# Kernel tuning notes

Measured on AMD Instinct MI355X. Metric: run time of the kernel, lower is better.

Reference implementation:

```python
import jax, jax.numpy as jnp
import numpy as np

EPS = 1e-6
N, D = 8192, 256


def setup_inputs() -> dict:
    key = jax.random.key(0)
    kq, kc = jax.random.split(key)
    # scale 0.05 keeps points inside the Poincare ball: c*||q||^2 ~ 0.06 << 1
    query = jax.random.normal(kq, (N, D), dtype=jnp.float32) * 0.05
    c = jnp.asarray(0.1, dtype=jnp.float32)  # learnable curvature param (init 0.1)
    return {"query": query, "c": c}


def reference(query, c):
    # Self-attention path of HyperbolicAttention (keys = values = query).
    clamp_c = jnp.maximum(c, EPS)
    # ||u-v||^2 = ||u||^2 + ||v||^2 - 2 u.v  (same math as explicit expand+subtract,
    # but via a single GEMM instead of an (N, N, D) intermediate)
    qn = jnp.sum(query * query, axis=-1)                       # (N,)
    gram = query @ query.T                                     # (N, N)
    diff_sq = jnp.maximum(qn[:, None] + qn[None, :] - 2.0 * gram, 0.0)
    t = jnp.maximum(1.0 - clamp_c * qn, EPS)                   # clamped 1 - c||x||^2
    denom = t[:, None] * t[None, :]                            # (N, N)
    arg = jnp.maximum(1.0 + 2.0 * clamp_c * diff_sq / denom, 1.0 + EPS) + EPS
    dist = jnp.arccosh(arg) / jnp.sqrt(clamp_c)                # (N, N)
    attn = jax.nn.softmax(-dist, axis=-1)                      # (N, N)
    return attn @ query                                        # (N, D)
```

## Files before the change

### kernel.cpp

```cpp
#include <hip/hip_runtime.h>
#include <math.h>

#define NN 8192
#define DD 256
#define EPSV 1e-6f
#define BM 128
#define BN 64
#define CSPLIT 4
#define COLS_PER_BLOCK (NN / CSPLIT)
#define NJT (COLS_PER_BLOCK / BN)
#define PSTR 72
#define TSTR 266
#define SMEM_BYTES (32768 * 3 + BM * PSTR * 2)

typedef __bf16 bf16x8 __attribute__((ext_vector_type(8)));
typedef float f32x16 __attribute__((ext_vector_type(16)));
typedef unsigned short ushort;
typedef unsigned int uint;


__device__ inline ushort f2bf(float x) {
    uint u = __float_as_uint(x);
    u += 0x7fffu + ((u >> 16) & 1u);
    return (ushort)(u >> 16);
}

__device__ inline void gload_lds16(const void* g, void* l) {
    __builtin_amdgcn_global_load_lds((const __attribute__((address_space(1))) uint*)g,
                                     (__attribute__((address_space(3))) uint*)l, 16, 0, 0);
}

__global__ void zero_kernel(float* __restrict__ p) {
    int i = blockIdx.x * 256 + threadIdx.x;
    ((float4*)p)[i] = make_float4(0.f, 0.f, 0.f, 0.f);
}

__global__ void prep_kernel(const float* __restrict__ q, const float* __restrict__ cp,
                            ushort* __restrict__ qbf, ushort* __restrict__ qbfT,
                            float* __restrict__ qn, float* __restrict__ itv2) {
    __shared__ ushort T[64 * TSTR];
    const int t = threadIdx.x;
    const int p0 = blockIdx.x * 64;
    const int pr = t >> 2, fq = t & 3;
    const int row = p0 + pr;
    const float4* src = (const float4*)(q + (size_t)row * DD + fq * 64);
    ushort loc[64];
    float ss = 0.f;
    #pragma unroll
    for (int i = 0; i < 16; ++i) {
        float4 v = src[i];
        ushort b0 = f2bf(v.x), b1 = f2bf(v.y), b2 = f2bf(v.z), b3 = f2bf(v.w);
        loc[i * 4 + 0] = b0; loc[i * 4 + 1] = b1; loc[i * 4 + 2] = b2; loc[i * 4 + 3] = b3;
        float r0 = __uint_as_float((uint)b0 << 16), r1 = __uint_as_float((uint)b1 << 16);
        float r2 = __uint_as_float((uint)b2 << 16), r3 = __uint_as_float((uint)b3 << 16);
        ss += r0 * r0 + r1 * r1 + r2 * r2 + r3 * r3;
    }
    #pragma unroll
    for (int k = 0; k < 8; ++k)
        *(uint4*)(qbf + (size_t)row * DD + (((fq * 8 + k) ^ (row & 7)) * 8)) = *(uint4*)&loc[k * 8];
    #pragma unroll
    for (int k = 0; k < 32; ++k)
        *(ushort2*)&T[pr * TSTR + fq * 64 + k * 2] = *(ushort2*)&loc[k * 2];
    ss += __shfl_xor(ss, 1, 64);
    ss += __shfl_xor(ss, 2, 64);
    if (fq == 0) {
        float cc = fmaxf(cp[0], EPSV);
        qn[row] = ss;
        float tt = fmaxf(1.0f - cc * ss, EPSV);
        itv2[row] = sqrtf(2.0f * cc) / tt;
    }
    __syncthreads();
    #pragma unroll
    for (int pass = 0; pass < 4; ++pass) {
        int f = pass * 64 + (t >> 2);
        int quarter = t & 3;
        ushort tmp[16];
        #pragma unroll
        for (int i = 0; i < 16; ++i) tmp[i] = T[(quarter * 16 + i) * TSTR + f];
        *(uint4*)(qbfT + (size_t)f * NN + p0 + quarter * 16) = *(uint4*)&tmp[0];
        *(uint4*)(qbfT + (size_t)f * NN + p0 + quarter * 16 + 8) = *(uint4*)&tmp[8];
    }
}

__global__ __launch_bounds__(512, 2) void flash_kernel(
    const ushort* __restrict__ qbf, const ushort* __restrict__ qbfT,
    const float* __restrict__ cp, const float* __restrict__ qn,
    const float* __restrict__ itv2, float* __restrict__ Oacc, float* __restrict__ lacc) {
    extern __shared__ char smem[];
    ushort* Ktlds = (ushort*)(smem + 65536);
    ushort* Plds = (ushort*)(smem + 98304);

    const int tid = threadIdx.x;
    const int lane = tid & 63;
    const int w = tid >> 6;
    const int l31 = lane & 31;
    const int lhi = lane >> 5;
    const int qr = w >> 1;
    const int qc = w & 1;
    const int R0 = blockIdx.y * BM;
    const int C0 = blockIdx.x * COLS_PER_BLOCK;

    const float cc = fmaxf(cp[0], EPSV);
    const float rsc = rsqrtf(cc);

    const int rowA = R0 + qr * 32 + l31;
    const ushort* qrow = qbf + (size_t)rowA * DD;
    bf16x8 qa[16];
    #pragma unroll
    for (int kk = 0; kk < 16; ++kk) {
        int c = kk * 2 + lhi;
        qa[kk] = *(const bf16x8*)(qrow + ((c ^ (rowA & 7)) * 8));
    }

    float qnr16[16], itr16[16];
    #pragma unroll
    for (int r = 0; r < 16; ++r) {
        int row = R0 + qr * 32 + (r & 3) + 8 * (r >> 2) + 4 * lhi;
        qnr16[r] = qn[row];
        itr16[r] = itv2[row];
    }

    f32x16 o[4];
    #pragma unroll
    for (int ct = 0; ct < 4; ++ct)
        #pragma unroll
        for (int i = 0; i < 16; ++i) o[ct][i] = 0.f;
    float racc[16];
    #pragma unroll
    for (int r = 0; r < 16; ++r) racc[r] = 0.f;

    {
        const char* g = (const char*)(qbf + (size_t)C0 * DD);
        #pragma unroll
        for (int i = 0; i < 4; ++i) {
            int base = i * 8192 + w * 1024;
            gload_lds16(g + base + lane * 16, smem + base);
        }
    }

    #pragma unroll 1
    for (int jt = 0; jt < NJT; ++jt) {
        const int C = C0 + jt * BN;
        const ushort* Kc = (const ushort*)(smem + (jt & 1) * 32768);
        __syncthreads();

        if (jt + 1 < NJT) {
            const char* g = (const char*)(qbf + (size_t)(C + BN) * DD);
            char* dst = smem + ((jt + 1) & 1) * 32768;
            #pragma unroll
            for (int i = 0; i < 4; ++i) {
                int base = i * 8192 + w * 1024;
                gload_lds16(g + base + lane * 16, dst + base);
            }
        }
        {
            #pragma unroll
            for (int i = 0; i < 4; ++i) {
                int f0 = i * 64 + w * 8;
                int f = f0 + (lane >> 3);
                const char* g = (const char*)(qbfT + (size_t)f * NN + C) +
                                (((lane & 7) ^ (f & 7)) * 16);
                gload_lds16(g, (char*)Ktlds + f0 * 128);
            }
        }

        f32x16 s;
        #pragma unroll
        for (int i = 0; i < 16; ++i) s[i] = 0.f;
        const int jrow = qc * 32 + l31;
        const ushort* krow = Kc + jrow * DD;
        #pragma unroll
        for (int kk = 0; kk < 16; ++kk) {
            int c = kk * 2 + lhi;
            bf16x8 b = *(const bf16x8*)(krow + ((c ^ (jrow & 7)) * 8));
            s = __builtin_amdgcn_mfma_f32_32x32x16_bf16(qa[kk], b, s, 0, 0, 0);
        }

        {
            int J = C + jrow;
            float qnj = qn[J];
            float itj = itv2[J];
            #pragma unroll
            for (int r = 0; r < 16; ++r) {
                int mloc = qr * 32 + (r & 3) + 8 * (r >> 2) + 4 * lhi;
                float diff = fmaxf(qnr16[r] + qnj - 2.0f * s[r], 0.0f);
                float u = diff * itr16[r] * itj;
                float z = fmaxf(1.0f + u, 1.0f + EPSV) + EPSV;
                float y = z + sqrtf(fmaf(z, z, -1.0f));
                float p = __builtin_amdgcn_exp2f(-rsc * __builtin_amdgcn_logf(y));
                racc[r] += p;
                Plds[mloc * PSTR + jrow] = f2bf(p);
            }
        }
        __syncthreads();

        #pragma unroll
        for (int kt = 0; kt < 4; ++kt) {
            bf16x8 pa = *(const bf16x8*)&Plds[(qr * 32 + l31) * PSTR + kt * 16 + 8 * lhi];
            #pragma unroll
            for (int ct = 0; ct < 4; ++ct) {
                int f = qc * 128 + ct * 32 + l31;
                int cj = kt * 2 + lhi;
                bf16x8 vb = *(const bf16x8*)(Ktlds + f * 64 + (((cj ^ (f & 7))) * 8));
                o[ct] = __builtin_amdgcn_mfma_f32_32x32x16_bf16(pa, vb, o[ct], 0, 0, 0);
            }
        }
    }

    #pragma unroll
    for (int ct = 0; ct < 4; ++ct) {
        #pragma unroll
        for (int r = 0; r < 16; ++r) {
            int row = R0 + qr * 32 + (r & 3) + 8 * (r >> 2) + 4 * lhi;
            int d = qc * 128 + ct * 32 + l31;
            atomicAdd(&Oacc[(size_t)row * DD + d], o[ct][r]);
        }
    }
    #pragma unroll
    for (int off = 1; off <= 16; off <<= 1)
        #pragma unroll
        for (int r = 0; r < 16; ++r) racc[r] += __shfl_xor(racc[r], off, 64);
    if (l31 == 0) {
        #pragma unroll
        for (int r = 0; r < 16; ++r) {
            int row = R0 + qr * 32 + (r & 3) + 8 * (r >> 2) + 4 * lhi;
            atomicAdd(&lacc[row], racc[r]);
        }
    }
}

__global__ void norm_kernel(const float* __restrict__ Oacc, const float* __restrict__ lacc,
                            float* __restrict__ out) {
    int i = blockIdx.x * 256 + threadIdx.x;
    float4 v = ((const float4*)Oacc)[i];
    float inv = 1.0f / lacc[i >> 6];
    ((float4*)out)[i] = make_float4(v.x * inv, v.y * inv, v.z * inv, v.w * inv);
}

extern "C" void kernel_launch(void* const* d_in, const int* in_sizes, int n_in,
                              void* d_out, int out_size, void* d_ws, size_t ws_size,
                              hipStream_t stream) {
    (void)in_sizes; (void)n_in; (void)out_size; (void)ws_size;
    const float* q = (const float*)d_in[0];
    const float* cp = (const float*)d_in[1];
    float* out = (float*)d_out;
    float* ws = (float*)d_ws;
    float* Oacc = ws;
    float* lacc = ws + (size_t)NN * DD;
    float* qn = lacc + NN;
    float* itv2 = qn + NN;
    ushort* qbf = (ushort*)(itv2 + NN);
    ushort* qbfT = qbf + (size_t)NN * DD;

    (void)hipFuncSetAttribute((const void*)flash_kernel,
                              hipFuncAttributeMaxDynamicSharedMemorySize, SMEM_BYTES);

    zero_kernel<<<(NN * DD + NN) / 4 / 256, 256, 0, stream>>>(ws);
    prep_kernel<<<NN / 64, 256, 0, stream>>>(q, cp, qbf, qbfT, qn, itv2);
    flash_kernel<<<dim3(CSPLIT, NN / BM), 512, SMEM_BYTES, stream>>>(qbf, qbfT, cp, qn, itv2, Oacc, lacc);
    norm_kernel<<<(NN * DD / 4) / 256, 256, 0, stream>>>(Oacc, lacc, out);
}
```

Before: 205.6 us.

## Pre-tile bf16 operands in MFMA fragment order and read K/V directly from global

The prep kernel now writes the bf16 query and its transpose in blocked layouts matching MFMA fragment order, packs the norm and inverse-t values into one float2 array, and zeroes the accumulators itself so the separate zero kernel goes away. The flash kernel drops the LDS staging of K and V and reads fragments straight from global memory (relying on cache), transposes the score GEMM so each lane owns one query row, and passes P through a smaller double-buffered LDS region built with lane shuffles, removing one barrier per tile. The aim is less LDS traffic, fewer barriers and one fewer launch. The risk is that uncoalesced or poorly cached global fragment loads now sit on the critical path without any prefetch overlap.

```diff
diff --git a/kernel.cpp b/kernel.cpp
--- a/kernel.cpp
+++ b/kernel.cpp
@@ -9,9 +9,7 @@
 #define CSPLIT 4
 #define COLS_PER_BLOCK (NN / CSPLIT)
 #define NJT (COLS_PER_BLOCK / BN)
-#define PSTR 72
 #define TSTR 266
-#define SMEM_BYTES (32768 * 3 + BM * PSTR * 2)
 
 typedef __bf16 bf16x8 __attribute__((ext_vector_type(8)));
 typedef float f32x16 __attribute__((ext_vector_type(16)));
@@ -25,24 +23,20 @@
     return (ushort)(u >> 16);
 }
 
-__device__ inline void gload_lds16(const void* g, void* l) {
-    __builtin_amdgcn_global_load_lds((const __attribute__((address_space(1))) uint*)g,
-                                     (__attribute__((address_space(3))) uint*)l, 16, 0, 0);
-}
-
-__global__ void zero_kernel(float* __restrict__ p) {
-    int i = blockIdx.x * 256 + threadIdx.x;
-    ((float4*)p)[i] = make_float4(0.f, 0.f, 0.f, 0.f);
-}
-
 __global__ void prep_kernel(const float* __restrict__ q, const float* __restrict__ cp,
-                            ushort* __restrict__ qbf, ushort* __restrict__ qbfT,
-                            float* __restrict__ qn, float* __restrict__ itv2) {
+                            ushort* __restrict__ qbfA, ushort* __restrict__ qbfB,
+                            float2* __restrict__ qni,
+                            float* __restrict__ Oacc, float* __restrict__ lacc) {
     __shared__ ushort T[64 * TSTR];
     const int t = threadIdx.x;
-    const int p0 = blockIdx.x * 64;
+    const int b = blockIdx.x;
+    float4 z4 = make_float4(0.f, 0.f, 0.f, 0.f);
+    #pragma unroll
+    for (int i = 0; i < 16; ++i) ((float4*)Oacc)[b * 4096 + i * 256 + t] = z4;
+    if (t < 16) ((float4*)lacc)[b * 16 + t] = z4;
+
     const int pr = t >> 2, fq = t & 3;
-    const int row = p0 + pr;
+    const int row = b * 64 + pr;
     const float4* src = (const float4*)(q + (size_t)row * DD + fq * 64);
     ushort loc[64];
     float ss = 0.f;
@@ -57,7 +51,7 @@
     }
     #pragma unroll
     for (int k = 0; k < 8; ++k)
-        *(uint4*)(qbf + (size_t)row * DD + (((fq * 8 + k) ^ (row & 7)) * 8)) = *(uint4*)&loc[k * 8];
+        *(uint4*)(qbfA + (((size_t)b * 32 + fq * 8 + k) * 64 + pr) * 8) = *(uint4*)&loc[k * 8];
     #pragma unroll
     for (int k = 0; k < 32; ++k)
         *(ushort2*)&T[pr * TSTR + fq * 64 + k * 2] = *(ushort2*)&loc[k * 2];
@@ -65,9 +59,8 @@
     ss += __shfl_xor(ss, 2, 64);
     if (fq == 0) {
         float cc = fmaxf(cp[0], EPSV);
-        qn[row] = ss;
         float tt = fmaxf(1.0f - cc * ss, EPSV);
-        itv2[row] = sqrtf(2.0f * cc) / tt;
+        qni[row] = make_float2(ss, sqrtf(2.0f * cc) / tt);
     }
     __syncthreads();
     #pragma unroll
@@ -77,156 +70,129 @@
         ushort tmp[16];
         #pragma unroll
         for (int i = 0; i < 16; ++i) tmp[i] = T[(quarter * 16 + i) * TSTR + f];
-        *(uint4*)(qbfT + (size_t)f * NN + p0 + quarter * 16) = *(uint4*)&tmp[0];
-        *(uint4*)(qbfT + (size_t)f * NN + p0 + quarter * 16 + 8) = *(uint4*)&tmp[8];
+        *(uint4*)(qbfB + (((size_t)b * 8 + quarter * 2 + 0) * 256 + f) * 8) = *(uint4*)&tmp[0];
+        *(uint4*)(qbfB + (((size_t)b * 8 + quarter * 2 + 1) * 256 + f) * 8) = *(uint4*)&tmp[8];
     }
 }
 
 __global__ __launch_bounds__(512, 2) void flash_kernel(
-    const ushort* __restrict__ qbf, const ushort* __restrict__ qbfT,
-    const float* __restrict__ cp, const float* __restrict__ qn,
-    const float* __restrict__ itv2, float* __restrict__ Oacc, float* __restrict__ lacc) {
-    extern __shared__ char smem[];
-    ushort* Ktlds = (ushort*)(smem + 65536);
-    ushort* Plds = (ushort*)(smem + 98304);
+    const ushort* __restrict__ qbfA, const ushort* __restrict__ qbfB,
+    const float* __restrict__ cp, const float2* __restrict__ qni,
+    float* __restrict__ Oacc, float* __restrict__ lacc) {
+    __shared__ char px[32768];
 
     const int tid = threadIdx.x;
     const int lane = tid & 63;
     const int w = tid >> 6;
     const int l31 = lane & 31;
     const int lhi = lane >> 5;
-    const int qr = w >> 1;
-    const int qc = w & 1;
-    const int R0 = blockIdx.y * BM;
-    const int C0 = blockIdx.x * COLS_PER_BLOCK;
+    const int mr = w >> 1;
+    const int jh = w & 1;
+
+    const int lid = blockIdx.x;
+    const int cs = lid & 3;
+    const int rb = lid >> 2;
+    const int R0 = rb * BM;
+    const int jbC0 = cs * (COLS_PER_BLOCK / 64);
 
     const float cc = fmaxf(cp[0], EPSV);
-    const float rsc = rsqrtf(cc);
-
-    const int rowA = R0 + qr * 32 + l31;
-    const ushort* qrow = qbf + (size_t)rowA * DD;
+    const float nrsc = -rsqrtf(cc);
+
     bf16x8 qa[16];
-    #pragma unroll
-    for (int kk = 0; kk < 16; ++kk) {
-        int c = kk * 2 + lhi;
-        qa[kk] = *(const bf16x8*)(qrow + ((c ^ (rowA & 7)) * 8));
-    }
-
-    float qnr16[16], itr16[16];
-    #pragma unroll
-    for (int r = 0; r < 16; ++r) {
-        int row = R0 + qr * 32 + (r & 3) + 8 * (r >> 2) + 4 * lhi;
-        qnr16[r] = qn[row];
-        itr16[r] = itv2[row];
-    }
+    {
+        const int jbQ = (R0 >> 6) + (mr >> 1);
+        const int rl = (mr & 1) * 32 + l31;
+        #pragma unroll
+        for (int kk = 0; kk < 16; ++kk)
+            qa[kk] = *(const bf16x8*)(qbfA + (((size_t)jbQ * 32 + kk * 2 + lhi) * 64 + rl) * 8);
+    }
+    const float2 mv = qni[R0 + mr * 32 + l31];
+    const float qn_m = mv.x, itv_m = mv.y;
 
     f32x16 o[4];
     #pragma unroll
-    for (int ct = 0; ct < 4; ++ct)
-        #pragma unroll
-        for (int i = 0; i < 16; ++i) o[ct][i] = 0.f;
-    float racc[16];
-    #pragma unroll
-    for (int r = 0; r < 16; ++r) racc[r] = 0.f;
-
-    {
-        const char* g = (const char*)(qbf + (size_t)C0 * DD);
-        #pragma unroll
-        for (int i = 0; i < 4; ++i) {
-            int base = i * 8192 + w * 1024;
-            gload_lds16(g + base + lane * 16, smem + base);
-        }
-    }
+    for (int ft = 0; ft < 4; ++ft)
+        #pragma unroll
+        for (int i = 0; i < 16; ++i) o[ft][i] = 0.f;
+    float racc = 0.f;
 
     #pragma unroll 1
     for (int jt = 0; jt < NJT; ++jt) {
-        const int C = C0 + jt * BN;
-        const ushort* Kc = (const ushort*)(smem + (jt & 1) * 32768);
+        const int jb = jbC0 + jt;
+        const int C = jb * 64;
+
+        f32x16 s;
+        #pragma unroll
+        for (int i = 0; i < 16; ++i) s[i] = 0.f;
+        #pragma unroll
+        for (int kk = 0; kk < 16; ++kk) {
+            bf16x8 kb = *(const bf16x8*)(qbfA + (((size_t)jb * 32 + kk * 2 + lhi) * 64 + jh * 32 + l31) * 8);
+            s = __builtin_amdgcn_mfma_f32_32x32x16_bf16(kb, qa[kk], s, 0, 0, 0);
+        }
+
+        float qnj[16], itj[16];
+        #pragma unroll
+        for (int rq = 0; rq < 4; ++rq) {
+            int j0 = C + jh * 32 + rq * 8 + 4 * lhi;
+            const float4* qp = (const float4*)(qni + j0);
+            float4 q01 = qp[0], q23 = qp[1];
+            qnj[rq * 4 + 0] = q01.x; itj[rq * 4 + 0] = q01.y;
+            qnj[rq * 4 + 1] = q01.z; itj[rq * 4 + 1] = q01.w;
+            qnj[rq * 4 + 2] = q23.x; itj[rq * 4 + 2] = q23.y;
+            qnj[rq * 4 + 3] = q23.z; itj[rq * 4 + 3] = q23.w;
+        }
+
+        float p[16];
+        #pragma unroll
+        for (int r = 0; r < 16; ++r) {
+            float diff = fmaf(-2.0f, s[r], qn_m + qnj[r]);
+            float z = fmaf(diff, itv_m * itj[r], 1.0f);
+            z = fmaxf(z, 1.0f + EPSV) + EPSV;
+            float y = z + sqrtf(fmaf(z, z, -1.0f));
+            float pv = __builtin_amdgcn_exp2f(nrsc * __builtin_amdgcn_logf(y));
+            racc += pv;
+            p[r] = pv;
+        }
+
+        float sh[16];
+        #pragma unroll
+        for (int r = 0; r < 16; ++r) sh[r] = __shfl_xor(p[r], 32, 64);
+        bf16x8 af0, af1;
+        #pragma unroll
+        for (int e = 0; e < 4; ++e) {
+            af0[e]     = (__bf16)(lhi ? sh[e + 4]  : p[e]);
+            af0[e + 4] = (__bf16)(lhi ? p[e + 4]  : sh[e]);
+            af1[e]     = (__bf16)(lhi ? sh[e + 12] : p[e + 8]);
+            af1[e + 4] = (__bf16)(lhi ? p[e + 12] : sh[e + 8]);
+        }
+
+        char* pxb = px + (jt & 1) * 16384;
+        *(bf16x8*)(pxb + ((mr * 4 + jh * 2 + 0) * 1024) + lane * 16) = af0;
+        *(bf16x8*)(pxb + ((mr * 4 + jh * 2 + 1) * 1024) + lane * 16) = af1;
         __syncthreads();
 
-        if (jt + 1 < NJT) {
-            const char* g = (const char*)(qbf + (size_t)(C + BN) * DD);
-            char* dst = smem + ((jt + 1) & 1) * 32768;
+        #pragma unroll
+        for (int kt = 0; kt < 4; ++kt) {
+            bf16x8 pa = *(const bf16x8*)(pxb + ((mr * 4 + kt) * 1024) + lane * 16);
             #pragma unroll
-            for (int i = 0; i < 4; ++i) {
-                int base = i * 8192 + w * 1024;
-                gload_lds16(g + base + lane * 16, dst + base);
+            for (int ft = 0; ft < 4; ++ft) {
+                bf16x8 vb = *(const bf16x8*)(qbfB +
+                    (((size_t)jb * 8 + kt * 2 + lhi) * 256 + jh * 128 + ft * 32 + l31) * 8);
+                o[ft] = __builtin_amdgcn_mfma_f32_32x32x16_bf16(pa, vb, o[ft], 0, 0, 0);
             }
         }
-        {
-            #pragma unroll
-            for (int i = 0; i < 4; ++i) {
-                int f0 = i * 64 + w * 8;
-                int f = f0 + (lane >> 3);
-                const char* g = (const char*)(qbfT + (size_t)f * NN + C) +
-                                (((lane & 7) ^ (f & 7)) * 16);
-                gload_lds16(g, (char*)Ktlds + f0 * 128);
-            }
-        }
-
-        f32x16 s;
-        #pragma unroll
-        for (int i = 0; i < 16; ++i) s[i] = 0.f;
-        const int jrow = qc * 32 + l31;
-        const ushort* krow = Kc + jrow * DD;
-        #pragma unroll
-        for (int kk = 0; kk < 16; ++kk) {
-            int c = kk * 2 + lhi;
-            bf16x8 b = *(const bf16x8*)(krow + ((c ^ (jrow & 7)) * 8));
-            s = __builtin_amdgcn_mfma_f32_32x32x16_bf16(qa[kk], b, s, 0, 0, 0);
-        }
-
-        {
-            int J = C + jrow;
-            float qnj = qn[J];
-            float itj = itv2[J];
-            #pragma unroll
-            for (int r = 0; r < 16; ++r) {
-                int mloc = qr * 32 + (r & 3) + 8 * (r >> 2) + 4 * lhi;
-                float diff = fmaxf(qnr16[r] + qnj - 2.0f * s[r], 0.0f);
-                float u = diff * itr16[r] * itj;
-                float z = fmaxf(1.0f + u, 1.0f + EPSV) + EPSV;
-                float y = z + sqrtf(fmaf(z, z, -1.0f));
-                float p = __builtin_amdgcn_exp2f(-rsc * __builtin_amdgcn_logf(y));
-                racc[r] += p;
-                Plds[mloc * PSTR + jrow] = f2bf(p);
-            }
-        }
-        __syncthreads();
-
-        #pragma unroll
-        for (int kt = 0; kt < 4; ++kt) {
-            bf16x8 pa = *(const bf16x8*)&Plds[(qr * 32 + l31) * PSTR + kt * 16 + 8 * lhi];
-            #pragma unroll
-            for (int ct = 0; ct < 4; ++ct) {
-                int f = qc * 128 + ct * 32 + l31;
-                int cj = kt * 2 + lhi;
-                bf16x8 vb = *(const bf16x8*)(Ktlds + f * 64 + (((cj ^ (f & 7))) * 8));
-                o[ct] = __builtin_amdgcn_mfma_f32_32x32x16_bf16(pa, vb, o[ct], 0, 0, 0);
-            }
-        }
-    }
-
-    #pragma unroll
-    for (int ct = 0; ct < 4; ++ct) {
+    }
+
+    #pragma unroll
+    for (int ft = 0; ft < 4; ++ft)
         #pragma unroll
         for (int r = 0; r < 16; ++r) {
-            int row = R0 + qr * 32 + (r & 3) + 8 * (r >> 2) + 4 * lhi;
-            int d = qc * 128 + ct * 32 + l31;
-            atomicAdd(&Oacc[(size_t)row * DD + d], o[ct][r]);
-        }
-    }
-    #pragma unroll
-    for (int off = 1; off <= 16; off <<= 1)
-        #pragma unroll
-        for (int r = 0; r < 16; ++r) racc[r] += __shfl_xor(racc[r], off, 64);
-    if (l31 == 0) {
-        #pragma unroll
-        for (int r = 0; r < 16; ++r) {
-            int row = R0 + qr * 32 + (r & 3) + 8 * (r >> 2) + 4 * lhi;
-            atomicAdd(&lacc[row], racc[r]);
-        }
-    }
+            int row = R0 + mr * 32 + (r & 3) + 8 * (r >> 2) + 4 * lhi;
+            int d = jh * 128 + ft * 32 + l31;
+            atomicAdd(&Oacc[(size_t)row * DD + d], o[ft][r]);
+        }
+    racc += __shfl_xor(racc, 32, 64);
+    if (lhi == 0) atomicAdd(&lacc[R0 + mr * 32 + l31], racc);
 }
 
 __global__ void norm_kernel(const float* __restrict__ Oacc, const float* __restrict__ lacc,
@@ -247,16 +213,11 @@
     float* ws = (float*)d_ws;
     float* Oacc = ws;
     float* lacc = ws + (size_t)NN * DD;
-    float* qn = lacc + NN;
-    float* itv2 = qn + NN;
-    ushort* qbf = (ushort*)(itv2 + NN);
-    ushort* qbfT = qbf + (size_t)NN * DD;
-
-    (void)hipFuncSetAttribute((const void*)flash_kernel,
-                              hipFuncAttributeMaxDynamicSharedMemorySize, SMEM_BYTES);
-
-    zero_kernel<<<(NN * DD + NN) / 4 / 256, 256, 0, stream>>>(ws);
-    prep_kernel<<<NN / 64, 256, 0, stream>>>(q, cp, qbf, qbfT, qn, itv2);
-    flash_kernel<<<dim3(CSPLIT, NN / BM), 512, SMEM_BYTES, stream>>>(qbf, qbfT, cp, qn, itv2, Oacc, lacc);
+    float2* qni = (float2*)(lacc + NN);
+    ushort* qbfA = (ushort*)(qni + NN);
+    ushort* qbfB = qbfA + (size_t)NN * DD;
+
+    prep_kernel<<<NN / 64, 256, 0, stream>>>(q, cp, qbfA, qbfB, qni, Oacc, lacc);
+    flash_kernel<<<CSPLIT * (NN / BM), 512, 0, stream>>>(qbfA, qbfB, cp, qni, Oacc, lacc);
     norm_kernel<<<(NN * DD / 4) / 256, 256, 0, stream>>>(Oacc, lacc, out);
 }
```

Result: slower. 289.4 us (+40.7%).
